# Optimization experiments

Measured on AMD Instinct MI355X. Metric: run time of the kernel, lower is better.

The kernel has to match this reference:

```python
import jax, jax.numpy as jnp
import numpy as np

D_MODEL = 1024
NUM_HEADS = 16
D_K = D_MODEL // NUM_HEADS


def setup_inputs() -> dict:
    key = jax.random.key(0)
    ks = jax.random.split(key, 7)
    B, S = 4, 2048
    lim = float(np.sqrt(6.0 / (D_MODEL + D_MODEL)))  # xavier uniform
    x = jax.random.normal(ks[0], (B, S, D_MODEL), dtype=jnp.float32)
    w_q = jax.random.uniform(ks[1], (D_MODEL, D_MODEL), jnp.float32, -lim, lim)
    w_k = jax.random.uniform(ks[2], (D_MODEL, D_MODEL), jnp.float32, -lim, lim)
    w_v = jax.random.uniform(ks[3], (D_MODEL, D_MODEL), jnp.float32, -lim, lim)
    w_o = jax.random.uniform(ks[4], (D_MODEL, D_MODEL), jnp.float32, -lim, lim)
    b_o = jnp.zeros((D_MODEL,), jnp.float32)
    ln_g = jnp.ones((D_MODEL,), jnp.float32)
    ln_b = jnp.zeros((D_MODEL,), jnp.float32)
    return {"x": x, "w_q": w_q, "w_k": w_k, "w_v": w_v, "w_o": w_o,
            "b_o": b_o, "ln_g": ln_g, "ln_b": ln_b}


def _layer_norm(y, g, b, eps=1e-5):
    mu = jnp.mean(y, axis=-1, keepdims=True)
    var = jnp.var(y, axis=-1, keepdims=True)
    return (y - mu) * jax.lax.rsqrt(var + eps) * g + b


def reference(x, w_q, w_k, w_v, w_o, b_o, ln_g, ln_b):
    B, S, D = x.shape
    # Linear weights stored torch-style [out, in]: y = x @ W^T
    def proj(w):
        return jnp.einsum('bsd,ed->bse', x, w).reshape(B, S, NUM_HEADS, D_K).transpose(0, 2, 1, 3)
    Q, K, V = proj(w_q), proj(w_k), proj(w_v)  # [B, H, S, d_k]
    scores = jnp.einsum('bhqd,bhkd->bhqk', Q, K) / jnp.sqrt(jnp.float32(D_K))
    attn = jax.nn.softmax(scores, axis=-1)  # dropout identity at eval
    out = jnp.einsum('bhqk,bhkd->bhqd', attn, V)  # [B, H, S, d_k]
    out = out.transpose(0, 2, 1, 3).reshape(B, S, D)
    out = jnp.einsum('bsd,ed->bse', out, w_o) + b_o
    return _layer_norm(x + out, ln_g, ln_b)
```

## Files before the change

### kernel.cpp

```cpp
#include <hip/hip_runtime.h>

typedef __bf16 bf16;
typedef bf16 v8bf __attribute__((ext_vector_type(8)));
typedef bf16 v4bf __attribute__((ext_vector_type(4)));
typedef float v4f __attribute__((ext_vector_type(4)));
typedef float v16f __attribute__((ext_vector_type(16)));
typedef unsigned int u32;
typedef u32 v4u __attribute__((ext_vector_type(4)));

#define GAS __attribute__((address_space(1)))
#define LAS __attribute__((address_space(3)))

constexpr int D    = 1024;
constexpr int ROWS = 8192;
constexpr int TILE = 128;

__global__ __launch_bounds__(256) void cast_all(
    const float* __restrict__ x,
    const float* __restrict__ wq, const float* __restrict__ wk,
    const float* __restrict__ wv, const float* __restrict__ wo,
    bf16* __restrict__ xb, bf16* __restrict__ wqb, bf16* __restrict__ wkb,
    bf16* __restrict__ wvb, bf16* __restrict__ wob)
{
    int i = blockIdx.x * 256 + threadIdx.x;
    const float* src; bf16* dst; int off;
    if (i < 2 * 1024 * 1024) { src = x; dst = xb; off = i; }
    else {
        int j = i - 2 * 1024 * 1024;
        int w = j >> 18;
        off = j & ((1 << 18) - 1);
        src = (w == 0) ? wq : (w == 1) ? wk : (w == 2) ? wv : wo;
        dst = (w == 0) ? wqb : (w == 1) ? wkb : (w == 2) ? wvb : wob;
    }
    float4 v = ((const float4*)src)[off];
    v4bf o;
    o[0] = (bf16)v.x; o[1] = (bf16)v.y; o[2] = (bf16)v.z; o[3] = (bf16)v.w;
    ((v4bf*)dst)[off] = o;
}

template<int MODE>
__global__ __launch_bounds__(256) void gemm_bt(
    const bf16* __restrict__ A,
    const bf16* __restrict__ W0, const bf16* __restrict__ W1, const bf16* __restrict__ W2,
    bf16* __restrict__ O0, bf16* __restrict__ O1, bf16* __restrict__ O2,
    float* __restrict__ Of, const float* __restrict__ bias,
    const float* __restrict__ X)
{
    __shared__ bf16 As[2][TILE * 32];
    __shared__ bf16 Bs[2][TILE * 32];

    const int tid  = threadIdx.x;
    const int lane = tid & 63;
    const int wave = tid >> 6;
    const int quad = lane >> 4;
    const int l16  = lane & 15;
    const int wm   = (wave >> 1) * 64;
    const int wn   = (wave & 1) * 64;

    const int z = blockIdx.z;
    const bf16* Bw = (MODE == 0) ? ((z == 0) ? W0 : ((z == 1) ? W1 : W2)) : W0;
    bf16*       Ob = (MODE == 0) ? ((z == 0) ? O0 : ((z == 1) ? O1 : O2)) : O0;

    const long rowA0 = (long)blockIdx.y * TILE;
    const long rowB0 = (long)blockIdx.x * TILE;

    const int stRow = wave * 16 + (lane >> 2);
    const int stCol = (lane & 3) * 8;
    const bf16* gA = A  + (rowA0 + stRow) * D + stCol;
    const bf16* gB = Bw + (rowB0 + stRow) * D + stCol;
    const int ldsOff = wave * 16 * 32;

    const v4f vzero = {0.f, 0.f, 0.f, 0.f};
    v4f acc[4][4];
    #pragma unroll
    for (int i = 0; i < 4; i++)
        #pragma unroll
        for (int j = 0; j < 4; j++) acc[i][j] = vzero;

    for (int k0 = 0; k0 < D; k0 += 64) {
        __syncthreads();
        #pragma unroll
        for (int p = 0; p < 2; ++p)
            #pragma unroll
            for (int i = 0; i < 2; ++i) {
                __builtin_amdgcn_global_load_lds(
                    (const GAS void*)(gA + (long)i * 64 * D + p * 32),
                    (LAS void*)(&As[p][ldsOff + i * 64 * 32]), 16, 0, 0);
                __builtin_amdgcn_global_load_lds(
                    (const GAS void*)(gB + (long)i * 64 * D + p * 32),
                    (LAS void*)(&Bs[p][ldsOff + i * 64 * 32]), 16, 0, 0);
            }
        gA += 64; gB += 64;
        __syncthreads();

        #pragma unroll
        for (int p = 0; p < 2; ++p) {
            v8bf a[4], b[4];
            #pragma unroll
            for (int mi = 0; mi < 4; mi++)
                a[mi] = *(const v8bf*)(&As[p][(wm + mi * 16 + l16) * 32 + quad * 8]);
            #pragma unroll
            for (int ni = 0; ni < 4; ni++)
                b[ni] = *(const v8bf*)(&Bs[p][(wn + ni * 16 + l16) * 32 + quad * 8]);
            #pragma unroll
            for (int mi = 0; mi < 4; mi++)
                #pragma unroll
                for (int ni = 0; ni < 4; ni++)
                    acc[mi][ni] = __builtin_amdgcn_mfma_f32_16x16x32_bf16(a[mi], b[ni], acc[mi][ni], 0, 0, 0);
        }
    }

    const float qscale = 0.125f * 1.44269504f;

    if (MODE == 0 && z == 2) {
        #pragma unroll
        for (int mi = 0; mi < 4; mi++) {
            #pragma unroll
            for (int ni = 0; ni < 4; ni++) {
                const long col = rowB0 + wn + ni * 16 + l16;
                const long h_ = col >> 6, dd = col & 63;
                const long row0 = rowA0 + wm + mi * 16 + quad * 4;
                const long b_ = row0 >> 11, s0 = row0 & 2047;
                v4bf pk;
                #pragma unroll
                for (int r = 0; r < 4; r++) pk[r] = (bf16)acc[mi][ni][r];
                *(v4bf*)(Ob + ((b_ * 16 + h_) * 64 + dd) * 2048 + s0) = pk;
            }
        }
    } else {
        #pragma unroll
        for (int mi = 0; mi < 4; mi++) {
            #pragma unroll
            for (int ni = 0; ni < 4; ni++) {
                const long col = rowB0 + wn + ni * 16 + l16;
                float bv = (MODE == 1) ? bias[col] : 0.f;
                #pragma unroll
                for (int r = 0; r < 4; r++) {
                    const long row = rowA0 + wm + mi * 16 + quad * 4 + r;
                    float v = acc[mi][ni][r];
                    if (MODE == 1) Of[row * D + col] = v + bv + X[row * D + col];
                    else {
                        if (z == 0) v *= qscale;
                        Ob[row * D + col] = (bf16)v;
                    }
                }
            }
        }
    }
}

__global__ __launch_bounds__(512, 4) void attn_kernel(
    const bf16* __restrict__ Q, const bf16* __restrict__ Kg,
    const bf16* __restrict__ VtG, bf16* __restrict__ O)
{
    const int id  = blockIdx.x;
    const int xcd = id & 7, j = id >> 3;
    const int qt  = j & 7;
    const int g   = xcd + 8 * (j >> 3);
    const int h   = g & 15, b = g >> 4;

    const int tid  = threadIdx.x;
    const int lane = tid & 63;
    const int wave = tid >> 6;
    const int l31  = lane & 31;
    const int hi   = lane >> 5;

    __shared__ bf16 Kt[4][64 * 64];
    __shared__ bf16 Vt[4][64 * 64];

    const long qrow = (long)(b * 2048 + qt * 256 + wave * 32 + l31);
    v8bf qB[4];
    #pragma unroll
    for (int f = 0; f < 4; f++)
        qB[f] = *(const v8bf*)(Q + qrow * D + h * 64 + f * 16 + hi * 8);

    const v16f z16 = {0.f,0.f,0.f,0.f,0.f,0.f,0.f,0.f,
                      0.f,0.f,0.f,0.f,0.f,0.f,0.f,0.f};
    v16f o_acc[2];
    o_acc[0] = z16; o_acc[1] = z16;
    float l0 = 0.f, l1 = 0.f;

    const int iR = tid >> 3;
    const int c8 = tid & 7;
    const bf16* kLane = Kg  + (long)b * 2048 * D + h * 64 + c8 * 8 + (long)iR * D;
    const bf16* vLane = VtG + (long)(b * 16 + h) * 64 * 2048 + c8 * 8 + (long)iR * 2048;
    const int wOff = iR * 64 + ((c8 ^ (iR & 7)) * 8);

    v8bf kp[2], vp[2];
    kp[0] = *(const v8bf*)(kLane); vp[0] = *(const v8bf*)(vLane);
    kLane += 64 * D; vLane += 64;
    kp[1] = *(const v8bf*)(kLane); vp[1] = *(const v8bf*)(vLane);
    kLane += 64 * D; vLane += 64;
    *(v8bf*)(&Kt[0][wOff]) = kp[0]; *(v8bf*)(&Vt[0][wOff]) = vp[0];
    *(v8bf*)(&Kt[1][wOff]) = kp[1]; *(v8bf*)(&Vt[1][wOff]) = vp[1];
    kp[0] = *(const v8bf*)(kLane); vp[0] = *(const v8bf*)(vLane);
    kLane += 64 * D; vLane += 64;
    kp[1] = *(const v8bf*)(kLane); vp[1] = *(const v8bf*)(vLane);
    kLane += 64 * D; vLane += 64;

    auto compute = [&](const int bq) {
        #pragma unroll
        for (int ko = 0; ko < 2; ko++) {
            const int krow = ko * 32 + l31;
            const int ksw  = krow & 7;
            v8bf kA[4];
            #pragma unroll
            for (int f = 0; f < 4; f++)
                kA[f] = *(const v8bf*)(&Kt[bq][krow * 64 + (((2 * f + hi) ^ ksw) * 8)]);
            __builtin_amdgcn_s_setprio(1);
            v16f st = __builtin_amdgcn_mfma_f32_32x32x16_bf16(kA[0], qB[0], z16, 0, 0, 0);
            st = __builtin_amdgcn_mfma_f32_32x32x16_bf16(kA[1], qB[1], st, 0, 0, 0);
            st = __builtin_amdgcn_mfma_f32_32x32x16_bf16(kA[2], qB[2], st, 0, 0, 0);
            st = __builtin_amdgcn_mfma_f32_32x32x16_bf16(kA[3], qB[3], st, 0, 0, 0);
            __builtin_amdgcn_s_setprio(0);

            float p[16];
            #pragma unroll
            for (int r = 0; r < 16; r++) {
                p[r] = __builtin_amdgcn_exp2f(st[r]);
                if (r & 1) l1 += p[r]; else l0 += p[r];
            }

            #pragma unroll
            for (int u = 0; u < 2; u++) {
                const int s = ko * 2 + u;
                u32 a0, a1, b0, b1;
                asm("v_cvt_pk_bf16_f32 %0, %1, %2" : "=v"(a0) : "v"(p[u*8+0]), "v"(p[u*8+1]));
                asm("v_cvt_pk_bf16_f32 %0, %1, %2" : "=v"(a1) : "v"(p[u*8+2]), "v"(p[u*8+3]));
                asm("v_cvt_pk_bf16_f32 %0, %1, %2" : "=v"(b0) : "v"(p[u*8+4]), "v"(p[u*8+5]));
                asm("v_cvt_pk_bf16_f32 %0, %1, %2" : "=v"(b1) : "v"(p[u*8+6]), "v"(p[u*8+7]));
                asm("v_permlane32_swap_b32 %0, %1" : "+v"(a0), "+v"(b0));
                asm("v_permlane32_swap_b32 %0, %1" : "+v"(a1), "+v"(b1));
                v4u w; w[0] = a0; w[1] = a1; w[2] = b0; w[3] = b1;
                const v8bf pa = __builtin_bit_cast(v8bf, w);
                const int vsw = (l31 & 7);
                v8bf vb0 = *(const v8bf*)(&Vt[bq][(l31)      * 64 + (((2 * s + hi) ^ vsw) * 8)]);
                v8bf vb1 = *(const v8bf*)(&Vt[bq][(32 + l31) * 64 + (((2 * s + hi) ^ vsw) * 8)]);
                __builtin_amdgcn_s_setprio(1);
                o_acc[0] = __builtin_amdgcn_mfma_f32_32x32x16_bf16(pa, vb0, o_acc[0], 0, 0, 0);
                o_acc[1] = __builtin_amdgcn_mfma_f32_32x32x16_bf16(pa, vb1, o_acc[1], 0, 0, 0);
                __builtin_amdgcn_s_setprio(0);
            }
        }
    };

    for (int gg = 0; gg < 16; ++gg) {
        const int cb = (gg & 1) * 2;
        __syncthreads();

        if (gg < 15) {
            *(v8bf*)(&Kt[cb ^ 2][wOff])       = kp[0];
            *(v8bf*)(&Vt[cb ^ 2][wOff])       = vp[0];
            *(v8bf*)(&Kt[(cb ^ 2) + 1][wOff]) = kp[1];
            *(v8bf*)(&Vt[(cb ^ 2) + 1][wOff]) = vp[1];
        }
        if (gg < 14) {
            kp[0] = *(const v8bf*)(kLane); vp[0] = *(const v8bf*)(vLane);
            kLane += 64 * D; vLane += 64;
            kp[1] = *(const v8bf*)(kLane); vp[1] = *(const v8bf*)(vLane);
            kLane += 64 * D; vLane += 64;
        }

        compute(cb);
        compute(cb + 1);
    }

    float l_acc = l0 + l1;
    l_acc += __shfl_xor(l_acc, 32);

    const long obase = (long)(b * 2048 + qt * 256 + wave * 32);
    #pragma unroll
    for (int r = 0; r < 16; r++) {
        const int qp = (r & 3) + 8 * (r >> 2) + 4 * hi;
        const float inv = 1.f / __shfl(l_acc, qp);
        O[(obase + qp) * D + h * 64 + l31]      = (bf16)(o_acc[0][r] * inv);
        O[(obase + qp) * D + h * 64 + 32 + l31] = (bf16)(o_acc[1][r] * inv);
    }
}

__global__ __launch_bounds__(256) void ln_kernel(
    const float* __restrict__ g, const float* __restrict__ beta,
    float* __restrict__ out)
{
    const int row = blockIdx.x;
    const int t = threadIdx.x;
    const int lane = t & 63, wave = t >> 6;
    const long base = (long)row * D + t * 4;

    float4 yv = *(const float4*)(out + base);
    float y0 = yv.x, y1 = yv.y, y2 = yv.z, y3 = yv.w;
    float s1 = y0 + y1 + y2 + y3;
    float s2 = y0*y0 + y1*y1 + y2*y2 + y3*y3;
    #pragma unroll
    for (int off = 1; off < 64; off <<= 1) {
        s1 += __shfl_xor(s1, off);
        s2 += __shfl_xor(s2, off);
    }
    __shared__ float r1[4], r2[4];
    if (lane == 0) { r1[wave] = s1; r2[wave] = s2; }
    __syncthreads();
    float S1 = r1[0] + r1[1] + r1[2] + r1[3];
    float S2 = r2[0] + r2[1] + r2[2] + r2[3];
    float mu  = S1 * (1.f / 1024.f);
    float var = S2 * (1.f / 1024.f) - mu * mu;
    float rsd = rsqrtf(var + 1e-5f);

    float4 gv = *(const float4*)(g + t * 4);
    float4 bv = *(const float4*)(beta + t * 4);
    float4 o;
    o.x = (y0 - mu) * rsd * gv.x + bv.x;
    o.y = (y1 - mu) * rsd * gv.y + bv.y;
    o.z = (y2 - mu) * rsd * gv.z + bv.z;
    o.w = (y3 - mu) * rsd * gv.w + bv.w;
    *(float4*)(out + base) = o;
}

extern "C" void kernel_launch(void* const* d_in, const int* in_sizes, int n_in,
                              void* d_out, int out_size, void* d_ws, size_t ws_size,
                              hipStream_t stream)
{
    const float* x   = (const float*)d_in[0];
    const float* wq  = (const float*)d_in[1];
    const float* wk  = (const float*)d_in[2];
    const float* wv  = (const float*)d_in[3];
    const float* wo  = (const float*)d_in[4];
    const float* bo  = (const float*)d_in[5];
    const float* lng = (const float*)d_in[6];
    const float* lnb = (const float*)d_in[7];
    float* out = (float*)d_out;

    char* ws = (char*)d_ws;
    bf16* xb  = (bf16*)(ws);
    bf16* wqb = (bf16*)(ws + (size_t)16 * 1024 * 1024);
    bf16* wkb = wqb + 1024 * 1024;
    bf16* wvb = wkb + 1024 * 1024;
    bf16* wob = wvb + 1024 * 1024;
    bf16* Qb  = (bf16*)(ws + (size_t)24 * 1024 * 1024);
    bf16* Kb  = Qb + (size_t)ROWS * D;
    bf16* VtG = Kb + (size_t)ROWS * D;
    bf16* Ab  = VtG + (size_t)ROWS * D;

    cast_all<<<12288, 256, 0, stream>>>(x, wq, wk, wv, wo,
                                        xb, wqb, wkb, wvb, wob);

    dim3 gqkv(D / TILE, ROWS / TILE, 3);
    gemm_bt<0><<<gqkv, 256, 0, stream>>>(xb, wqb, wkb, wvb, Qb, Kb, VtG,
                                         nullptr, nullptr, nullptr);

    attn_kernel<<<dim3(512, 1, 1), 512, 0, stream>>>(Qb, Kb, VtG, Ab);

    dim3 gout(D / TILE, ROWS / TILE, 1);
    gemm_bt<1><<<gout, 256, 0, stream>>>(Ab, wob, nullptr, nullptr,
                                         nullptr, nullptr, nullptr, out, bo, x);

    ln_kernel<<<8192, 256, 0, stream>>>(lng, lnb, out);
}
```

Measured before the change: 298.9 us.

## Replace GEMMs with 256x128 tiles, swizzled LDS and triple-buffered pipeline

The projection and output GEMMs are rewritten as one kernel, gemm8, with 512-thread blocks and 256x128 output tiles. It uses K=64 stages held in XOR-swizzled LDS, triple buffering with explicit vmcnt waits, and raised wave priority around the MFMA blocks. The QKV projection now treats the three contiguous weight matrices as one 3072-wide N dimension, so Q, K and V run in a single flat grid. Block IDs are remapped so that tiles sharing the same rows land on the same XCD. The goal is better operand reuse, fewer barriers and overlap of global-to-LDS loads with MFMA work. The cost is about 144KB of LDS per block, which limits occupancy to one block per CU, and a dependence on the weight buffers being adjacent in the workspace.

```diff
diff --git a/kernel.cpp b/kernel.cpp
--- a/kernel.cpp
+++ b/kernel.cpp
@@ -13,7 +13,6 @@
 
 constexpr int D    = 1024;
 constexpr int ROWS = 8192;
-constexpr int TILE = 128;
 
 __global__ __launch_bounds__(256) void cast_all(
     const float* __restrict__ x,
@@ -38,16 +37,22 @@
     ((v4bf*)dst)[off] = o;
 }
 
-template<int MODE>
-__global__ __launch_bounds__(256) void gemm_bt(
-    const bf16* __restrict__ A,
-    const bf16* __restrict__ W0, const bf16* __restrict__ W1, const bf16* __restrict__ W2,
-    bf16* __restrict__ O0, bf16* __restrict__ O1, bf16* __restrict__ O2,
+template<int MODE, int NTN>
+__global__ __launch_bounds__(512, 2) void gemm8(
+    const bf16* __restrict__ A, const bf16* __restrict__ W,
+    bf16* __restrict__ Oq, bf16* __restrict__ Ok, bf16* __restrict__ Ov,
     float* __restrict__ Of, const float* __restrict__ bias,
     const float* __restrict__ X)
 {
-    __shared__ bf16 As[2][TILE * 32];
-    __shared__ bf16 Bs[2][TILE * 32];
+    __shared__ bf16 Abuf[3][256 * 64];
+    __shared__ bf16 Bbuf[3][128 * 64];
+
+    const int id   = blockIdx.x;
+    const int wgid = (id & 7) * (4 * NTN) + (id >> 3);
+    const int mT   = wgid / NTN;
+    const int nT   = wgid - mT * NTN;
+    const long rowA0 = (long)mT * 256;
+    const long colB0 = (long)nT * 128;
 
     const int tid  = threadIdx.x;
     const int lane = tid & 63;
@@ -57,18 +62,26 @@
     const int wm   = (wave >> 1) * 64;
     const int wn   = (wave & 1) * 64;
 
-    const int z = blockIdx.z;
-    const bf16* Bw = (MODE == 0) ? ((z == 0) ? W0 : ((z == 1) ? W1 : W2)) : W0;
-    bf16*       Ob = (MODE == 0) ? ((z == 0) ? O0 : ((z == 1) ? O1 : O2)) : O0;
-
-    const long rowA0 = (long)blockIdx.y * TILE;
-    const long rowB0 = (long)blockIdx.x * TILE;
-
-    const int stRow = wave * 16 + (lane >> 2);
-    const int stCol = (lane & 3) * 8;
-    const bf16* gA = A  + (rowA0 + stRow) * D + stCol;
-    const bf16* gB = Bw + (rowB0 + stRow) * D + stCol;
-    const int ldsOff = wave * 16 * 32;
+    const int srow = wave * 8 + (lane >> 3);
+    const int scol = ((lane & 7) ^ (lane >> 3)) * 8;
+    const bf16* gA = A + (rowA0 + srow) * D + scol;
+    const bf16* gB = W + (colB0 + srow) * D + scol;
+    const int dstOff = wave * 512;
+
+    auto stage = [&](int bi, int t) {
+        const bf16* a = gA + (long)t * 64;
+        const bf16* b = gB + (long)t * 64;
+        #pragma unroll
+        for (int i = 0; i < 4; i++)
+            __builtin_amdgcn_global_load_lds(
+                (const GAS void*)(a + (long)i * 64 * D),
+                (LAS void*)(&Abuf[bi][i * 4096 + dstOff]), 16, 0, 0);
+        #pragma unroll
+        for (int i = 0; i < 2; i++)
+            __builtin_amdgcn_global_load_lds(
+                (const GAS void*)(b + (long)i * 64 * D),
+                (LAS void*)(&Bbuf[bi][i * 4096 + dstOff]), 16, 0, 0);
+    };
 
     const v4f vzero = {0.f, 0.f, 0.f, 0.f};
     v4f acc[4][4];
@@ -77,54 +90,85 @@
         #pragma unroll
         for (int j = 0; j < 4; j++) acc[i][j] = vzero;
 
-    for (int k0 = 0; k0 < D; k0 += 64) {
-        __syncthreads();
-        #pragma unroll
-        for (int p = 0; p < 2; ++p)
-            #pragma unroll
-            for (int i = 0; i < 2; ++i) {
-                __builtin_amdgcn_global_load_lds(
-                    (const GAS void*)(gA + (long)i * 64 * D + p * 32),
-                    (LAS void*)(&As[p][ldsOff + i * 64 * 32]), 16, 0, 0);
-                __builtin_amdgcn_global_load_lds(
-                    (const GAS void*)(gB + (long)i * 64 * D + p * 32),
-                    (LAS void*)(&Bs[p][ldsOff + i * 64 * 32]), 16, 0, 0);
-            }
-        gA += 64; gB += 64;
-        __syncthreads();
-
-        #pragma unroll
-        for (int p = 0; p < 2; ++p) {
-            v8bf a[4], b[4];
+    int sa[2], sb[2];
+    #pragma unroll
+    for (int ks = 0; ks < 2; ks++) {
+        const int ch = ((ks * 4 + quad) ^ (l16 & 7)) * 8;
+        sa[ks] = (wm + l16) * 64 + ch;
+        sb[ks] = (wn + l16) * 64 + ch;
+    }
+
+    auto compute = [&](int bi) {
+        const bf16* As = &Abuf[bi][0];
+        const bf16* Bs = &Bbuf[bi][0];
+        v8bf af[2][4], bf[2][4];
+        #pragma unroll
+        for (int ks = 0; ks < 2; ks++) {
             #pragma unroll
             for (int mi = 0; mi < 4; mi++)
-                a[mi] = *(const v8bf*)(&As[p][(wm + mi * 16 + l16) * 32 + quad * 8]);
+                af[ks][mi] = *(const v8bf*)(As + sa[ks] + mi * 1024);
             #pragma unroll
             for (int ni = 0; ni < 4; ni++)
-                b[ni] = *(const v8bf*)(&Bs[p][(wn + ni * 16 + l16) * 32 + quad * 8]);
+                bf[ks][ni] = *(const v8bf*)(Bs + sb[ks] + ni * 1024);
+        }
+        __builtin_amdgcn_s_setprio(1);
+        #pragma unroll
+        for (int ks = 0; ks < 2; ks++)
             #pragma unroll
             for (int mi = 0; mi < 4; mi++)
                 #pragma unroll
                 for (int ni = 0; ni < 4; ni++)
-                    acc[mi][ni] = __builtin_amdgcn_mfma_f32_16x16x32_bf16(a[mi], b[ni], acc[mi][ni], 0, 0, 0);
+                    acc[mi][ni] = __builtin_amdgcn_mfma_f32_16x16x32_bf16(
+                        af[ks][mi], bf[ks][ni], acc[mi][ni], 0, 0, 0);
+        __builtin_amdgcn_s_setprio(0);
+    };
+
+    constexpr int NT = 16;
+    stage(0, 0);
+    stage(1, 1);
+    asm volatile("s_waitcnt vmcnt(6)" ::: "memory");
+    __builtin_amdgcn_s_barrier();
+
+    for (int t = 0; t < NT; ++t) {
+        if (t + 2 < NT) stage((t + 2) % 3, t + 2);
+        compute(t % 3);
+        if (t + 1 < NT) {
+            if (t + 2 < NT) {
+                asm volatile("s_waitcnt vmcnt(6)" ::: "memory");
+            } else {
+                asm volatile("s_waitcnt vmcnt(0)" ::: "memory");
+            }
+            __builtin_amdgcn_s_barrier();
         }
     }
 
     const float qscale = 0.125f * 1.44269504f;
 
-    if (MODE == 0 && z == 2) {
+    if (MODE == 0) {
+        const int z = (int)(colB0 >> 10);
         #pragma unroll
         for (int mi = 0; mi < 4; mi++) {
             #pragma unroll
             for (int ni = 0; ni < 4; ni++) {
-                const long col = rowB0 + wn + ni * 16 + l16;
-                const long h_ = col >> 6, dd = col & 63;
+                const long col = colB0 + wn + ni * 16 + l16;
+                const long c   = col & 1023;
                 const long row0 = rowA0 + wm + mi * 16 + quad * 4;
-                const long b_ = row0 >> 11, s0 = row0 & 2047;
-                v4bf pk;
-                #pragma unroll
-                for (int r = 0; r < 4; r++) pk[r] = (bf16)acc[mi][ni][r];
-                *(v4bf*)(Ob + ((b_ * 16 + h_) * 64 + dd) * 2048 + s0) = pk;
+                if (z == 2) {
+                    const long h_ = c >> 6, dd = c & 63;
+                    const long b_ = row0 >> 11, s0 = row0 & 2047;
+                    v4bf pk;
+                    #pragma unroll
+                    for (int r = 0; r < 4; r++) pk[r] = (bf16)acc[mi][ni][r];
+                    *(v4bf*)(Ov + ((b_ * 16 + h_) * 64 + dd) * 2048 + s0) = pk;
+                } else {
+                    bf16* Ob = (z == 0) ? Oq : Ok;
+                    #pragma unroll
+                    for (int r = 0; r < 4; r++) {
+                        float v = acc[mi][ni][r];
+                        if (z == 0) v *= qscale;
+                        Ob[(row0 + r) * D + c] = (bf16)v;
+                    }
+                }
             }
         }
     } else {
@@ -132,17 +176,12 @@
         for (int mi = 0; mi < 4; mi++) {
             #pragma unroll
             for (int ni = 0; ni < 4; ni++) {
-                const long col = rowB0 + wn + ni * 16 + l16;
-                float bv = (MODE == 1) ? bias[col] : 0.f;
+                const long col = colB0 + wn + ni * 16 + l16;
+                const float bv = bias[col];
                 #pragma unroll
                 for (int r = 0; r < 4; r++) {
                     const long row = rowA0 + wm + mi * 16 + quad * 4 + r;
-                    float v = acc[mi][ni][r];
-                    if (MODE == 1) Of[row * D + col] = v + bv + X[row * D + col];
-                    else {
-                        if (z == 0) v *= qscale;
-                        Ob[row * D + col] = (bf16)v;
-                    }
+                    Of[row * D + col] = acc[mi][ni][r] + bv + X[row * D + col];
                 }
             }
         }
@@ -343,15 +382,13 @@
     cast_all<<<12288, 256, 0, stream>>>(x, wq, wk, wv, wo,
                                         xb, wqb, wkb, wvb, wob);
 
-    dim3 gqkv(D / TILE, ROWS / TILE, 3);
-    gemm_bt<0><<<gqkv, 256, 0, stream>>>(xb, wqb, wkb, wvb, Qb, Kb, VtG,
-                                         nullptr, nullptr, nullptr);
+    gemm8<0, 24><<<768, 512, 0, stream>>>(xb, wqb, Qb, Kb, VtG,
+                                          nullptr, nullptr, nullptr);
 
     attn_kernel<<<dim3(512, 1, 1), 512, 0, stream>>>(Qb, Kb, VtG, Ab);
 
-    dim3 gout(D / TILE, ROWS / TILE, 1);
-    gemm_bt<1><<<gout, 256, 0, stream>>>(Ab, wob, nullptr, nullptr,
-                                         nullptr, nullptr, nullptr, out, bo, x);
+    gemm8<1, 8><<<256, 512, 0, stream>>>(Ab, wob, nullptr, nullptr, nullptr,
+                                         out, bo, x);
 
     ln_kernel<<<8192, 256, 0, stream>>>(lng, lnb, out);
 }
```

Result: no change. 299.8 us (+0.3%).
